# Kernel tuning notes

Hardware: AMD Instinct MI355X
Metric: run time of the kernel (lower is better)

The kernel has to match this reference:

```python
import jax, jax.numpy as jnp
import numpy as np
import math

B, S, D = 2, 2048, 1024
H = 16
HD = D // H
SPARSITY = 0.8


def setup_inputs() -> dict:
    key = jax.random.key(0)
    ks = jax.random.split(key, 5)
    scale = 1.0 / math.sqrt(D)
    return {
        "hidden_states": jax.random.normal(ks[0], (B, S, D), dtype=jnp.float32),
        "Wq": jax.random.normal(ks[1], (D, D), dtype=jnp.float32) * scale,
        "bq": jnp.zeros((D,), dtype=jnp.float32),
        "Wk": jax.random.normal(ks[2], (D, D), dtype=jnp.float32) * scale,
        "bk": jnp.zeros((D,), dtype=jnp.float32),
        "Wv": jax.random.normal(ks[3], (D, D), dtype=jnp.float32) * scale,
        "bv": jnp.zeros((D,), dtype=jnp.float32),
        "Wo": jax.random.normal(ks[4], (D, D), dtype=jnp.float32) * scale,
        "bo": jnp.zeros((D,), dtype=jnp.float32),
    }


def reference(hidden_states, Wq, bq, Wk, bk, Wv, bv, Wo, bo):
    b, s, d = hidden_states.shape
    # projections (torch Linear: x @ W.T + b), split heads -> [b, h, s, hd]
    def proj(W, bias):
        y = hidden_states @ W.T + bias
        return y.reshape(b, s, H, HD).transpose(0, 2, 1, 3)

    q = proj(Wq, bq)
    k = proj(Wk, bk)
    v = proj(Wv, bv)

    # scaled dot-product scores [b, h, s, s]
    attn = jnp.einsum("bhqd,bhkd->bhqk", q, k) / math.sqrt(HD)

    # top-k threshold per query row (k-th largest == sort-descending[k-1])
    kk = max(int(s * (1.0 - SPARSITY)), 1)
    thr = jax.lax.top_k(attn, kk)[0][..., kk - 1:kk]  # [b, h, s, 1]
    attn = attn + jnp.where(attn < thr, jnp.float32(-10000.0), jnp.float32(0.0))

    attn = jax.nn.softmax(attn, axis=-1)
    out = jnp.einsum("bhqk,bhkd->bhqd", attn, v)  # [b, h, s, hd]
    out = out.transpose(0, 2, 1, 3).reshape(b, s, d)
    return out @ Wo.T + bo
```

## Files before the change

### kernel.cpp

```cpp
#include <hip/hip_runtime.h>
#include <math.h>

#define S_LEN 2048
#define NH 16
#define HDIM 64
#define BATCH 2
#define BHC 32
#define KK 409
#define DMODEL 1024

typedef __attribute__((ext_vector_type(8))) short bf16x8;
typedef __attribute__((ext_vector_type(4))) float f32x4;

#define SC_STR 1032
#define P_STR  2056
#define T_STR  40

__device__ __forceinline__ unsigned f2ord(float f) {
    unsigned u = __float_as_uint(f);
    return (u & 0x80000000u) ? ~u : (u | 0x80000000u);
}
__device__ __forceinline__ float ord2f(unsigned v) {
    unsigned u = (v & 0x80000000u) ? (v & 0x7fffffffu) : ~v;
    return __uint_as_float(u);
}
__device__ __forceinline__ unsigned short f2bf(float f) {
    unsigned u = __float_as_uint(f);
    u += 0x7fffu + ((u >> 16) & 1u);
    return (unsigned short)(u >> 16);
}
__device__ __forceinline__ float bf2f(unsigned short h) {
    return __uint_as_float(((unsigned)h) << 16);
}

__global__ __launch_bounds__(256)
void split32(const float* __restrict__ in, unsigned short* __restrict__ hi,
             unsigned short* __restrict__ lo, int n4)
{
    const int i = blockIdx.x * 256 + threadIdx.x;
    if (i < n4) {
        const float4 v = ((const float4*)in)[i];
        ushort4 h, l;
        h.x = f2bf(v.x); l.x = f2bf(v.x - bf2f(h.x));
        h.y = f2bf(v.y); l.y = f2bf(v.y - bf2f(h.y));
        h.z = f2bf(v.z); l.z = f2bf(v.z - bf2f(h.z));
        h.w = f2bf(v.w); l.w = f2bf(v.w - bf2f(h.w));
        ((ushort4*)hi)[i] = h;
        ((ushort4*)lo)[i] = l;
    }
}

__global__ __launch_bounds__(256)
void gemm_mfma(const unsigned short* __restrict__ Ah, const unsigned short* __restrict__ Al,
               const unsigned short* __restrict__ Bh, const unsigned short* __restrict__ Bl,
               const float* __restrict__ bias, void* __restrict__ out0,
               void* __restrict__ out1, int mode)
{
    __shared__ __align__(16) unsigned short sAh[128 * T_STR];
    __shared__ __align__(16) unsigned short sAl[128 * T_STR];
    __shared__ __align__(16) unsigned short sBh[64 * T_STR];
    __shared__ __align__(16) unsigned short sBl[64 * T_STR];

    const int tid  = threadIdx.x;
    const int lane = tid & 63;
    const int w    = tid >> 6;
    const int q15  = lane & 15;
    const int quad = lane >> 4;
    const int n0b = blockIdx.x * 64;
    const int m0b = blockIdx.y * 128;
    const int wm = (w >> 1) * 64;
    const int wn = (w & 1) * 32;

    const int ar0 = tid >> 2, aks0 = (tid & 3) * 8;
    const int ar1 = (tid + 256) >> 2, aks1 = aks0;
    const int br = tid >> 2, bks = (tid & 3) * 8;

    const unsigned short* gAh0 = Ah + (size_t)(m0b + ar0) * 1024 + aks0;
    const unsigned short* gAh1 = Ah + (size_t)(m0b + ar1) * 1024 + aks1;
    const unsigned short* gAl0 = Al + (size_t)(m0b + ar0) * 1024 + aks0;
    const unsigned short* gAl1 = Al + (size_t)(m0b + ar1) * 1024 + aks1;
    const unsigned short* gBh = Bh + (size_t)(n0b + br) * 1024 + bks;
    const unsigned short* gBl = Bl + (size_t)(n0b + br) * 1024 + bks;

    f32x4 acc[4][2];
#pragma unroll
    for (int mt = 0; mt < 4; ++mt)
#pragma unroll
        for (int nt = 0; nt < 2; ++nt) acc[mt][nt] = (f32x4){0.f, 0.f, 0.f, 0.f};

#pragma unroll 1
    for (int k0 = 0; k0 < 1024; k0 += 32) {
        const bf16x8 vah0 = *(const bf16x8*)(gAh0 + k0);
        const bf16x8 vah1 = *(const bf16x8*)(gAh1 + k0);
        const bf16x8 val0 = *(const bf16x8*)(gAl0 + k0);
        const bf16x8 val1 = *(const bf16x8*)(gAl1 + k0);
        const bf16x8 vbh  = *(const bf16x8*)(gBh + k0);
        const bf16x8 vbl  = *(const bf16x8*)(gBl + k0);
        __syncthreads();
        *(bf16x8*)(sAh + ar0 * T_STR + aks0) = vah0;
        *(bf16x8*)(sAh + ar1 * T_STR + aks1) = vah1;
        *(bf16x8*)(sAl + ar0 * T_STR + aks0) = val0;
        *(bf16x8*)(sAl + ar1 * T_STR + aks1) = val1;
        *(bf16x8*)(sBh + br * T_STR + bks) = vbh;
        *(bf16x8*)(sBl + br * T_STR + bks) = vbl;
        __syncthreads();

        bf16x8 fbh[2], fbl[2];
#pragma unroll
        for (int nt = 0; nt < 2; ++nt) {
            fbh[nt] = *(const bf16x8*)(sBh + (wn + nt * 16 + q15) * T_STR + quad * 8);
            fbl[nt] = *(const bf16x8*)(sBl + (wn + nt * 16 + q15) * T_STR + quad * 8);
        }
#pragma unroll
        for (int mt = 0; mt < 4; ++mt) {
            const bf16x8 fah = *(const bf16x8*)(sAh + (wm + mt * 16 + q15) * T_STR + quad * 8);
            const bf16x8 fal = *(const bf16x8*)(sAl + (wm + mt * 16 + q15) * T_STR + quad * 8);
#pragma unroll
            for (int nt = 0; nt < 2; ++nt) {
                acc[mt][nt] = __builtin_amdgcn_mfma_f32_16x16x32_bf16(fah, fbh[nt], acc[mt][nt], 0, 0, 0);
                acc[mt][nt] = __builtin_amdgcn_mfma_f32_16x16x32_bf16(fah, fbl[nt], acc[mt][nt], 0, 0, 0);
                acc[mt][nt] = __builtin_amdgcn_mfma_f32_16x16x32_bf16(fal, fbh[nt], acc[mt][nt], 0, 0, 0);
            }
        }
    }

#pragma unroll
    for (int nt = 0; nt < 2; ++nt) {
        const int n = n0b + wn + nt * 16 + q15;
        const float bv = bias[n];
#pragma unroll
        for (int mt = 0; mt < 4; ++mt) {
            const int mb = m0b + wm + mt * 16 + quad * 4;
#pragma unroll
            for (int rg = 0; rg < 4; ++rg) {
                const int m = mb + rg;
                const float o = acc[mt][nt][rg] + bv;
                if (mode == 0) {
                    ((float*)out0)[(size_t)m * 1024 + n] = o;
                } else {
                    const int b = m >> 11, s = m & 2047;
                    const int h = n >> 6, hd = n & 63;
                    const size_t base = ((size_t)((b * NH + h) * S_LEN + s)) * HDIM + hd;
                    if (mode == 3) {
                        ((unsigned short*)out0)[base] = f2bf(o);
                    } else {
                        const unsigned short oh = f2bf(o);
                        ((unsigned short*)out0)[base] = oh;
                        ((unsigned short*)out1)[base] = f2bf(o - bf2f(oh));
                    }
                }
            }
        }
    }
}

__global__ __launch_bounds__(256)
void transpose_v16(const unsigned short* __restrict__ V, unsigned short* __restrict__ Vt)
{
    __shared__ unsigned short t[64][72];
    const int tid = threadIdx.x;
    const int s0 = blockIdx.x * 64;
    const int bh = blockIdx.y;
    const unsigned short* Vb = V + (size_t)bh * S_LEN * HDIM;
#pragma unroll
    for (int i = 0; i < 4; ++i) {
        const int f = tid + i * 256;
        const int s = f >> 4;
        const int hq = (f & 15) * 4;
        const ushort4 v = *(const ushort4*)(Vb + (size_t)(s0 + s) * HDIM + hq);
        t[s][hq + 0] = v.x; t[s][hq + 1] = v.y; t[s][hq + 2] = v.z; t[s][hq + 3] = v.w;
    }
    __syncthreads();
    unsigned short* Vtb = Vt + (size_t)bh * HDIM * S_LEN;
#pragma unroll
    for (int i = 0; i < 4; ++i) {
        const int f = tid + i * 256;
        const int hd = f >> 4;
        const int sq = (f & 15) * 4;
        ushort4 v;
        v.x = t[sq + 0][hd]; v.y = t[sq + 1][hd];
        v.z = t[sq + 2][hd]; v.w = t[sq + 3][hd];
        *(ushort4*)(Vtb + (size_t)hd * S_LEN + s0 + sq) = v;
    }
}

__device__ __forceinline__ unsigned radix_select(const unsigned* u)
{
    unsigned T = 0;
    int rem = KK;
    int C = 2048;
#pragma unroll 1
    for (int b = 31; b >= 0; --b) {
        const unsigned want = (T >> b) | 1u;
        int cnt = 0;
#pragma unroll
        for (int i = 0; i < 32; ++i)
            cnt += __builtin_popcountll(__ballot((u[i] >> b) == want));
        if (cnt >= rem) { T |= (1u << b); C = cnt; }
        else { rem -= cnt; C -= cnt; }
        if (C == rem) {
            const unsigned pre = T >> b;
            unsigned mn = 0xffffffffu;
#pragma unroll
            for (int i = 0; i < 32; ++i) {
                const unsigned v = ((u[i] >> b) == pre) ? u[i] : 0xffffffffu;
                mn = v < mn ? v : mn;
            }
#pragma unroll
            for (int off = 32; off >= 1; off >>= 1) {
                const unsigned o = (unsigned)__shfl_xor((int)mn, off);
                mn = o < mn ? o : mn;
            }
            return mn;
        }
    }
    return T;
}

__global__ __launch_bounds__(512, 4)
void attn_kernel(const unsigned short* __restrict__ Qh, const unsigned short* __restrict__ Ql,
                 const unsigned short* __restrict__ Kh, const unsigned short* __restrict__ Kl,
                 const unsigned short* __restrict__ Vt,
                 unsigned short* __restrict__ AOh, unsigned short* __restrict__ AOl)
{
    extern __shared__ __align__(16) char smem[];
    float* sc = (float*)smem;
    unsigned short* P = (unsigned short*)smem;
    float* Opart = (float*)smem;

    const int tid  = threadIdx.x;
    const int lane = tid & 63;
    const int w    = tid >> 6;
    const int q15  = lane & 15;
    const int quad = lane >> 4;

    const int blk = blockIdx.x;
    const int bh  = (blk & 7) * 4 + ((blk >> 3) & 3);
    const int q0  = (blk >> 5) * 16;

    const size_t qrow = ((size_t)bh * S_LEN + q0 + q15) * HDIM;
    const bf16x8 bqh0 = *(const bf16x8*)(Qh + qrow + quad * 8);
    const bf16x8 bqh1 = *(const bf16x8*)(Qh + qrow + 32 + quad * 8);
    const bf16x8 bql0 = *(const bf16x8*)(Ql + qrow + quad * 8);
    const bf16x8 bql1 = *(const bf16x8*)(Ql + qrow + 32 + quad * 8);

    const size_t kbase = (size_t)bh * S_LEN * HDIM;
    const int r0 = 2 * w, r1 = 2 * w + 1;
    unsigned u0[32], u1[32];

#pragma unroll 1
    for (int half = 0; half < 2; ++half) {
        f32x4 acc[8];
#pragma unroll 2
        for (int t = 0; t < 8; ++t) {
            const int key = w * 256 + half * 128 + t * 16 + q15;
            const unsigned short* kh = Kh + kbase + (size_t)key * HDIM + quad * 8;
            const unsigned short* kl = Kl + kbase + (size_t)key * HDIM + quad * 8;
            const bf16x8 akh0 = *(const bf16x8*)(kh);
            const bf16x8 akh1 = *(const bf16x8*)(kh + 32);
            const bf16x8 akl0 = *(const bf16x8*)(kl);
            const bf16x8 akl1 = *(const bf16x8*)(kl + 32);
            f32x4 c = {0.f, 0.f, 0.f, 0.f};
            c = __builtin_amdgcn_mfma_f32_16x16x32_bf16(akh0, bqh0, c, 0, 0, 0);
            c = __builtin_amdgcn_mfma_f32_16x16x32_bf16(akh1, bqh1, c, 0, 0, 0);
            c = __builtin_amdgcn_mfma_f32_16x16x32_bf16(akh0, bql0, c, 0, 0, 0);
            c = __builtin_amdgcn_mfma_f32_16x16x32_bf16(akh1, bql1, c, 0, 0, 0);
            c = __builtin_amdgcn_mfma_f32_16x16x32_bf16(akl0, bqh0, c, 0, 0, 0);
            c = __builtin_amdgcn_mfma_f32_16x16x32_bf16(akl1, bqh1, c, 0, 0, 0);
            acc[t] = c * 0.125f;
        }
        if (half) __syncthreads();
#pragma unroll
        for (int t = 0; t < 8; ++t)
            *(f32x4*)(sc + q15 * SC_STR + w * 128 + t * 16 + quad * 4) = acc[t];
        __syncthreads();
        unsigned* d0 = u0 + half * 16;
        unsigned* d1 = u1 + half * 16;
#pragma unroll
        for (int i = 0; i < 16; ++i) d0[i] = f2ord(sc[r0 * SC_STR + i * 64 + lane]);
#pragma unroll
        for (int i = 0; i < 16; ++i) d1[i] = f2ord(sc[r1 * SC_STR + i * 64 + lane]);
    }
    __syncthreads();

    float invd[2];
#pragma unroll 1
    for (int rr = 0; rr < 2; ++rr) {
        const unsigned* u = rr ? u1 : u0;
        const int r = rr ? r1 : r0;
        const unsigned T = radix_select(u);
        unsigned umx = 0;
#pragma unroll
        for (int i = 0; i < 32; ++i) umx = u[i] > umx ? u[i] : umx;
#pragma unroll
        for (int off = 32; off >= 1; off >>= 1) {
            const unsigned o = (unsigned)__shfl_xor((int)umx, off);
            umx = o > umx ? o : umx;
        }
        const float mx = ord2f(umx);
        float lsum = 0.f;
        unsigned short* Pr = P + r * P_STR;
#pragma unroll
        for (int i = 0; i < 32; ++i) {
            const int ii = i & 15;
            const int kb = ii * 64 + (ii >> 1) * 128 + (i >> 4) * 128;
            const float e = (u[i] >= T) ? __expf(ord2f(u[i]) - mx) : 0.f;
            Pr[kb + lane] = f2bf(e);
            lsum += e;
        }
#pragma unroll
        for (int off = 32; off >= 1; off >>= 1) lsum += __shfl_xor(lsum, off);
        invd[rr] = 1.f / lsum;
    }
    __syncthreads();

    {
        f32x4 oacc[4];
#pragma unroll
        for (int ht = 0; ht < 4; ++ht) oacc[ht] = (f32x4){0.f, 0.f, 0.f, 0.f};
        const size_t vtb = (size_t)bh * HDIM * S_LEN;
#pragma unroll 2
        for (int ks = 0; ks < 8; ++ks) {
            const int key0 = w * 256 + ks * 32 + quad * 8;
            const bf16x8 ap = *(const bf16x8*)(P + q15 * P_STR + key0);
#pragma unroll
            for (int ht = 0; ht < 4; ++ht) {
                const int hd = ht * 16 + q15;
                const bf16x8 bv = *(const bf16x8*)(Vt + vtb + (size_t)hd * S_LEN + key0);
                oacc[ht] = __builtin_amdgcn_mfma_f32_16x16x32_bf16(ap, bv, oacc[ht], 0, 0, 0);
            }
        }
        __syncthreads();
#pragma unroll
        for (int ht = 0; ht < 4; ++ht)
#pragma unroll
            for (int rg = 0; rg < 4; ++rg)
                Opart[w * 1024 + (quad * 4 + rg) * 64 + ht * 16 + q15] = oacc[ht][rg];
    }
    __syncthreads();

    {
        float s0 = 0.f, s1 = 0.f;
#pragma unroll
        for (int ww = 0; ww < 8; ++ww) {
            s0 += Opart[ww * 1024 + r0 * 64 + lane];
            s1 += Opart[ww * 1024 + r1 * 64 + lane];
        }
        const int b = bh >> 4, h = bh & 15;
        const float o0 = s0 * invd[0];
        const float o1 = s1 * invd[1];
        const size_t i0 = ((size_t)(b * S_LEN + q0 + r0)) * DMODEL + h * HDIM + lane;
        const size_t i1 = ((size_t)(b * S_LEN + q0 + r1)) * DMODEL + h * HDIM + lane;
        const unsigned short h0 = f2bf(o0), h1 = f2bf(o1);
        AOh[i0] = h0; AOl[i0] = f2bf(o0 - bf2f(h0));
        AOh[i1] = h1; AOl[i1] = f2bf(o1 - bf2f(h1));
    }
}

extern "C" void kernel_launch(void* const* d_in, const int* in_sizes, int n_in,
                              void* d_out, int out_size, void* d_ws, size_t ws_size,
                              hipStream_t stream)
{
    const float* X  = (const float*)d_in[0];
    const float* Wq = (const float*)d_in[1];
    const float* bq = (const float*)d_in[2];
    const float* Wk = (const float*)d_in[3];
    const float* bk = (const float*)d_in[4];
    const float* Wv = (const float*)d_in[5];
    const float* bv = (const float*)d_in[6];
    const float* Wo = (const float*)d_in[7];
    const float* bo = (const float*)d_in[8];

    char* p = (char*)d_ws;
    const size_t NEL = (size_t)BHC * S_LEN * HDIM;
    unsigned short* Q16h = (unsigned short*)p; p += NEL * 2;
    unsigned short* Q16l = (unsigned short*)p; p += NEL * 2;
    unsigned short* K16h = (unsigned short*)p; p += NEL * 2;
    unsigned short* K16l = (unsigned short*)p; p += NEL * 2;
    unsigned short* Vb16 = (unsigned short*)p; p += NEL * 2;
    unsigned short* Vt16 = (unsigned short*)p; p += NEL * 2;
    unsigned short* Xh   = (unsigned short*)p; p += NEL * 2;
    unsigned short* Xl   = (unsigned short*)p; p += NEL * 2;
    unsigned short* AOh  = (unsigned short*)p; p += NEL * 2;
    unsigned short* AOl  = (unsigned short*)p; p += NEL * 2;
    unsigned short* Wqh  = (unsigned short*)p; p += DMODEL * DMODEL * 2;
    unsigned short* Wql  = (unsigned short*)p; p += DMODEL * DMODEL * 2;
    unsigned short* Wkh  = (unsigned short*)p; p += DMODEL * DMODEL * 2;
    unsigned short* Wkl  = (unsigned short*)p; p += DMODEL * DMODEL * 2;
    unsigned short* Wvh  = (unsigned short*)p; p += DMODEL * DMODEL * 2;
    unsigned short* Wvl  = (unsigned short*)p; p += DMODEL * DMODEL * 2;
    unsigned short* Woh  = (unsigned short*)p; p += DMODEL * DMODEL * 2;
    unsigned short* Wol  = (unsigned short*)p; p += DMODEL * DMODEL * 2;

    const int attn_lds = 16 * SC_STR * 4;
    hipFuncSetAttribute((const void*)attn_kernel,
                        hipFuncAttributeMaxDynamicSharedMemorySize, attn_lds);

    const int X4 = (int)(NEL / 4);
    const int W4 = DMODEL * DMODEL / 4;

    split32<<<(X4 + 255) / 256, 256, 0, stream>>>(X,  Xh,  Xl,  X4);
    split32<<<(W4 + 255) / 256, 256, 0, stream>>>(Wq, Wqh, Wql, W4);
    split32<<<(W4 + 255) / 256, 256, 0, stream>>>(Wk, Wkh, Wkl, W4);
    split32<<<(W4 + 255) / 256, 256, 0, stream>>>(Wv, Wvh, Wvl, W4);
    split32<<<(W4 + 255) / 256, 256, 0, stream>>>(Wo, Woh, Wol, W4);

    const dim3 ggrid(16, 32, 1);
    gemm_mfma<<<ggrid, 256, 0, stream>>>(Xh, Xl, Wqh, Wql, bq, Q16h, Q16l, 2);
    gemm_mfma<<<ggrid, 256, 0, stream>>>(Xh, Xl, Wkh, Wkl, bk, K16h, K16l, 2);
    gemm_mfma<<<ggrid, 256, 0, stream>>>(Xh, Xl, Wvh, Wvl, bv, Vb16, nullptr, 3);
    transpose_v16<<<dim3(32, 32, 1), 256, 0, stream>>>(Vb16, Vt16);

    attn_kernel<<<4096, 512, attn_lds, stream>>>(Q16h, Q16l, K16h, K16l, Vt16, AOh, AOl);

    gemm_mfma<<<ggrid, 256, 0, stream>>>(AOh, AOl, Woh, Wol, bo, d_out, nullptr, 0);
}
```

Measured before the change: 859.6 us.

## Use 16 waves per attention block, one query row per wave

```diff
diff --git a/kernel.cpp b/kernel.cpp
--- a/kernel.cpp
+++ b/kernel.cpp
@@ -12,9 +12,9 @@
 typedef __attribute__((ext_vector_type(8))) short bf16x8;
 typedef __attribute__((ext_vector_type(4))) float f32x4;
 
-#define SC_STR 1032
-#define P_STR  2056
-#define T_STR  40
+#define SC_STRW 2056
+#define P_STR   2064
+#define T_STR   40
 
 __device__ __forceinline__ unsigned f2ord(float f) {
     unsigned u = __float_as_uint(f);
@@ -184,7 +184,7 @@
     }
 }
 
-__device__ __forceinline__ unsigned radix_select(const unsigned* u)
+__device__ __forceinline__ unsigned radix_select(const unsigned (&u)[32])
 {
     unsigned T = 0;
     int rem = KK;
@@ -217,7 +217,7 @@
     return T;
 }
 
-__global__ __launch_bounds__(512, 4)
+__global__ __launch_bounds__(1024, 4)
 void attn_kernel(const unsigned short* __restrict__ Qh, const unsigned short* __restrict__ Ql,
                  const unsigned short* __restrict__ Kh, const unsigned short* __restrict__ Kl,
                  const unsigned short* __restrict__ Vt,
@@ -226,7 +226,7 @@
     extern __shared__ __align__(16) char smem[];
     float* sc = (float*)smem;
     unsigned short* P = (unsigned short*)smem;
-    float* Opart = (float*)smem;
+    float* Opart = (float*)(smem + 66048);
 
     const int tid  = threadIdx.x;
     const int lane = tid & 63;
@@ -235,8 +235,10 @@
     const int quad = lane >> 4;
 
     const int blk = blockIdx.x;
-    const int bh  = (blk & 7) * 4 + ((blk >> 3) & 3);
-    const int q0  = (blk >> 5) * 16;
+    const int xcd = blk & 7;
+    const int j   = blk >> 3;
+    const int bh  = xcd * 4 + (j >> 7);
+    const int q0  = (j & 127) * 16;
 
     const size_t qrow = ((size_t)bh * S_LEN + q0 + q15) * HDIM;
     const bf16x8 bqh0 = *(const bf16x8*)(Qh + qrow + quad * 8);
@@ -245,73 +247,53 @@
     const bf16x8 bql1 = *(const bf16x8*)(Ql + qrow + 32 + quad * 8);
 
     const size_t kbase = (size_t)bh * S_LEN * HDIM;
-    const int r0 = 2 * w, r1 = 2 * w + 1;
-    unsigned u0[32], u1[32];
-
-#pragma unroll 1
-    for (int half = 0; half < 2; ++half) {
-        f32x4 acc[8];
+
 #pragma unroll 2
-        for (int t = 0; t < 8; ++t) {
-            const int key = w * 256 + half * 128 + t * 16 + q15;
-            const unsigned short* kh = Kh + kbase + (size_t)key * HDIM + quad * 8;
-            const unsigned short* kl = Kl + kbase + (size_t)key * HDIM + quad * 8;
-            const bf16x8 akh0 = *(const bf16x8*)(kh);
-            const bf16x8 akh1 = *(const bf16x8*)(kh + 32);
-            const bf16x8 akl0 = *(const bf16x8*)(kl);
-            const bf16x8 akl1 = *(const bf16x8*)(kl + 32);
-            f32x4 c = {0.f, 0.f, 0.f, 0.f};
-            c = __builtin_amdgcn_mfma_f32_16x16x32_bf16(akh0, bqh0, c, 0, 0, 0);
-            c = __builtin_amdgcn_mfma_f32_16x16x32_bf16(akh1, bqh1, c, 0, 0, 0);
-            c = __builtin_amdgcn_mfma_f32_16x16x32_bf16(akh0, bql0, c, 0, 0, 0);
-            c = __builtin_amdgcn_mfma_f32_16x16x32_bf16(akh1, bql1, c, 0, 0, 0);
-            c = __builtin_amdgcn_mfma_f32_16x16x32_bf16(akl0, bqh0, c, 0, 0, 0);
-            c = __builtin_amdgcn_mfma_f32_16x16x32_bf16(akl1, bqh1, c, 0, 0, 0);
-            acc[t] = c * 0.125f;
-        }
-        if (half) __syncthreads();
-#pragma unroll
-        for (int t = 0; t < 8; ++t)
-            *(f32x4*)(sc + q15 * SC_STR + w * 128 + t * 16 + quad * 4) = acc[t];
-        __syncthreads();
-        unsigned* d0 = u0 + half * 16;
-        unsigned* d1 = u1 + half * 16;
-#pragma unroll
-        for (int i = 0; i < 16; ++i) d0[i] = f2ord(sc[r0 * SC_STR + i * 64 + lane]);
-#pragma unroll
-        for (int i = 0; i < 16; ++i) d1[i] = f2ord(sc[r1 * SC_STR + i * 64 + lane]);
-    }
-    __syncthreads();
-
-    float invd[2];
-#pragma unroll 1
-    for (int rr = 0; rr < 2; ++rr) {
-        const unsigned* u = rr ? u1 : u0;
-        const int r = rr ? r1 : r0;
-        const unsigned T = radix_select(u);
-        unsigned umx = 0;
-#pragma unroll
-        for (int i = 0; i < 32; ++i) umx = u[i] > umx ? u[i] : umx;
-#pragma unroll
-        for (int off = 32; off >= 1; off >>= 1) {
-            const unsigned o = (unsigned)__shfl_xor((int)umx, off);
-            umx = o > umx ? o : umx;
-        }
-        const float mx = ord2f(umx);
-        float lsum = 0.f;
-        unsigned short* Pr = P + r * P_STR;
-#pragma unroll
-        for (int i = 0; i < 32; ++i) {
-            const int ii = i & 15;
-            const int kb = ii * 64 + (ii >> 1) * 128 + (i >> 4) * 128;
-            const float e = (u[i] >= T) ? __expf(ord2f(u[i]) - mx) : 0.f;
-            Pr[kb + lane] = f2bf(e);
-            lsum += e;
-        }
-#pragma unroll
-        for (int off = 32; off >= 1; off >>= 1) lsum += __shfl_xor(lsum, off);
-        invd[rr] = 1.f / lsum;
-    }
+    for (int t = 0; t < 8; ++t) {
+        const int key = w * 128 + t * 16 + q15;
+        const unsigned short* kh = Kh + kbase + (size_t)key * HDIM + quad * 8;
+        const unsigned short* kl = Kl + kbase + (size_t)key * HDIM + quad * 8;
+        const bf16x8 akh0 = *(const bf16x8*)(kh);
+        const bf16x8 akh1 = *(const bf16x8*)(kh + 32);
+        const bf16x8 akl0 = *(const bf16x8*)(kl);
+        const bf16x8 akl1 = *(const bf16x8*)(kl + 32);
+        f32x4 c = {0.f, 0.f, 0.f, 0.f};
+        c = __builtin_amdgcn_mfma_f32_16x16x32_bf16(akh0, bqh0, c, 0, 0, 0);
+        c = __builtin_amdgcn_mfma_f32_16x16x32_bf16(akh1, bqh1, c, 0, 0, 0);
+        c = __builtin_amdgcn_mfma_f32_16x16x32_bf16(akh0, bql0, c, 0, 0, 0);
+        c = __builtin_amdgcn_mfma_f32_16x16x32_bf16(akh1, bql1, c, 0, 0, 0);
+        c = __builtin_amdgcn_mfma_f32_16x16x32_bf16(akl0, bqh0, c, 0, 0, 0);
+        c = __builtin_amdgcn_mfma_f32_16x16x32_bf16(akl1, bqh1, c, 0, 0, 0);
+        *(f32x4*)(sc + q15 * SC_STRW + w * 128 + t * 16 + quad * 4) = c * 0.125f;
+    }
+    __syncthreads();
+
+    unsigned u[32];
+#pragma unroll
+    for (int i = 0; i < 32; ++i) u[i] = f2ord(sc[w * SC_STRW + i * 64 + lane]);
+    __syncthreads();
+
+    const unsigned T = radix_select(u);
+    unsigned umx = 0;
+#pragma unroll
+    for (int i = 0; i < 32; ++i) umx = u[i] > umx ? u[i] : umx;
+#pragma unroll
+    for (int off = 32; off >= 1; off >>= 1) {
+        const unsigned o = (unsigned)__shfl_xor((int)umx, off);
+        umx = o > umx ? o : umx;
+    }
+    const float mx = ord2f(umx);
+    float lsum = 0.f;
+    unsigned short* Pr = P + w * P_STR;
+#pragma unroll
+    for (int i = 0; i < 32; ++i) {
+        const float e = (u[i] >= T) ? __expf(ord2f(u[i]) - mx) : 0.f;
+        Pr[i * 64 + lane] = f2bf(e);
+        lsum += e;
+    }
+#pragma unroll
+    for (int off = 32; off >= 1; off >>= 1) lsum += __shfl_xor(lsum, off);
+    const float invd = 1.f / lsum;
     __syncthreads();
 
     {
@@ -319,9 +301,9 @@
 #pragma unroll
         for (int ht = 0; ht < 4; ++ht) oacc[ht] = (f32x4){0.f, 0.f, 0.f, 0.f};
         const size_t vtb = (size_t)bh * HDIM * S_LEN;
-#pragma unroll 2
-        for (int ks = 0; ks < 8; ++ks) {
-            const int key0 = w * 256 + ks * 32 + quad * 8;
+#pragma unroll
+        for (int ks = 0; ks < 4; ++ks) {
+            const int key0 = w * 128 + ks * 32 + quad * 8;
             const bf16x8 ap = *(const bf16x8*)(P + q15 * P_STR + key0);
 #pragma unroll
             for (int ht = 0; ht < 4; ++ht) {
@@ -330,7 +312,6 @@
                 oacc[ht] = __builtin_amdgcn_mfma_f32_16x16x32_bf16(ap, bv, oacc[ht], 0, 0, 0);
             }
         }
-        __syncthreads();
 #pragma unroll
         for (int ht = 0; ht < 4; ++ht)
 #pragma unroll
@@ -340,20 +321,15 @@
     __syncthreads();
 
     {
-        float s0 = 0.f, s1 = 0.f;
-#pragma unroll
-        for (int ww = 0; ww < 8; ++ww) {
-            s0 += Opart[ww * 1024 + r0 * 64 + lane];
-            s1 += Opart[ww * 1024 + r1 * 64 + lane];
-        }
+        float s = 0.f;
+#pragma unroll
+        for (int ww = 0; ww < 16; ++ww) s += Opart[ww * 1024 + w * 64 + lane];
+        const float o = s * invd;
         const int b = bh >> 4, h = bh & 15;
-        const float o0 = s0 * invd[0];
-        const float o1 = s1 * invd[1];
-        const size_t i0 = ((size_t)(b * S_LEN + q0 + r0)) * DMODEL + h * HDIM + lane;
-        const size_t i1 = ((size_t)(b * S_LEN + q0 + r1)) * DMODEL + h * HDIM + lane;
-        const unsigned short h0 = f2bf(o0), h1 = f2bf(o1);
-        AOh[i0] = h0; AOl[i0] = f2bf(o0 - bf2f(h0));
-        AOh[i1] = h1; AOl[i1] = f2bf(o1 - bf2f(h1));
+        const size_t idx = ((size_t)(b * S_LEN + q0 + w)) * DMODEL + h * HDIM + lane;
+        const unsigned short hh = f2bf(o);
+        AOh[idx] = hh;
+        AOl[idx] = f2bf(o - bf2f(hh));
     }
 }
 
@@ -392,7 +368,7 @@
     unsigned short* Woh  = (unsigned short*)p; p += DMODEL * DMODEL * 2;
     unsigned short* Wol  = (unsigned short*)p; p += DMODEL * DMODEL * 2;
 
-    const int attn_lds = 16 * SC_STR * 4;
+    const int attn_lds = 16 * SC_STRW * 4;
     hipFuncSetAttribute((const void*)attn_kernel,
                         hipFuncAttributeMaxDynamicSharedMemorySize, attn_lds);
 
@@ -411,7 +387,7 @@
     gemm_mfma<<<ggrid, 256, 0, stream>>>(Xh, Xl, Wvh, Wvl, bv, Vb16, nullptr, 3);
     transpose_v16<<<dim3(32, 32, 1), 256, 0, stream>>>(Vb16, Vt16);
 
-    attn_kernel<<<4096, 512, attn_lds, stream>>>(Q16h, Q16l, K16h, K16l, Vt16, AOh, AOl);
+    attn_kernel<<<4096, 1024, attn_lds, stream>>>(Q16h, Q16l, K16h, K16l, Vt16, AOh, AOl);
 
     gemm_mfma<<<ggrid, 256, 0, stream>>>(AOh, AOl, Woh, Wol, bo, d_out, nullptr, 0);
 }
```

Result: slower. 943.5 us (+9.8%).
